# Kernel optimization log

Hardware: AMD Instinct MI355X
Metric: run time of the kernel (lower is better)

The kernel has to match this reference:

```python
import jax, jax.numpy as jnp
import numpy as np
from jax import lax

D = 768          # embed_dim
H = 12           # n_heads
DEPTH = 2
T = 6            # n_timepoints
PS = 7           # patch_size
IMG = (56, 49, 49)
GRID = (8, 7, 7)
NPATCH = 392     # prod(GRID), must be even for the sinusoidal PE
SEQ = T * NPATCH # 2352 space-time tokens
MLP_H = 3072     # int(768 * 4.0)
B = 2
RRELU_MLP = 0.4        # eval-mode RReLU(0.1, 0.7) slope
RRELU_HEAD = 11.0/48.0 # eval-mode RReLU(1/8, 1/3) slope


def _ln(x, g, b, eps=1e-6):
    m = x.mean(-1, keepdims=True)
    v = ((x - m) ** 2).mean(-1, keepdims=True)
    return (x - m) / jnp.sqrt(v + eps) * g + b


def _pos_enc(t, d):
    pos = np.arange(t, dtype=np.float32)[:, None]
    div = 1.0 / 10000.0 ** (np.arange(0, d, 2, dtype=np.float32) / d)
    pe = np.zeros((t, d), np.float32)
    pe[:, 0::2] = np.sin(pos * div)
    pe[:, 1::2] = np.cos(pos * div)
    return jnp.asarray(pe)


def _convT_dw(x, w, bias, stride, dilation):
    # depthwise ConvTranspose3d(C, C, k, stride, dilation, groups=C); w: (C,1,k,k,k)
    C = x.shape[1]
    k = w.shape[-1]
    wf = jnp.flip(w, axis=(2, 3, 4))
    pad = (k - 1) * dilation
    y = lax.conv_general_dilated(
        x, wf, window_strides=(1, 1, 1), padding=[(pad, pad)] * 3,
        lhs_dilation=(stride,) * 3, rhs_dilation=(dilation,) * 3,
        dimension_numbers=('NCDHW', 'OIDHW', 'NCDHW'), feature_group_count=C)
    return y + bias[None, :, None, None, None]


def _nearest(x, size):
    # torch F.interpolate(mode='nearest'): src = floor(dst * in/out)
    for ax, s in zip((2, 3, 4), size):
        idx = (jnp.arange(s) * (x.shape[ax] / s)).astype(jnp.int32)
        x = jnp.take(x, idx, axis=ax)
    return x


def setup_inputs() -> dict:
    key = jax.random.key(0)
    ks = iter(jax.random.split(key, 64))
    def rn(shape, s=0.02):
        return jax.random.normal(next(ks), shape, jnp.float32) * s
    inp = {}
    inp['x'] = jax.random.normal(next(ks), (B, 1, T) + IMG, jnp.float32)
    inp['pconv_w'] = rn((D, 1, PS, PS, PS)); inp['pconv_b'] = rn((D,))
    inp['pos_embed'] = rn((1, SEQ, D))
    inp['ln1_g'] = jnp.ones((DEPTH, D)); inp['ln1_b'] = jnp.zeros((DEPTH, D))
    inp['qkv_w'] = rn((DEPTH, 3 * D, D)); inp['qkv_b'] = rn((DEPTH, 3 * D))
    inp['proj_w'] = rn((DEPTH, D, D)); inp['proj_b'] = rn((DEPTH, D))
    inp['ln2_g'] = jnp.ones((DEPTH, D)); inp['ln2_b'] = jnp.zeros((DEPTH, D))
    inp['fc1_w'] = rn((DEPTH, MLP_H, D)); inp['fc1_b'] = rn((DEPTH, MLP_H))
    inp['fc2_w'] = rn((DEPTH, D, MLP_H)); inp['fc2_b'] = rn((DEPTH, D))
    inp['normf_g'] = jnp.ones((D,)); inp['normf_b'] = jnp.zeros((D,))
    inp['dfc_w'] = rn((1, D)); inp['dfc_b'] = rn((1,))
    inp['up1_w'] = rn((T, 1, 7, 7, 7)); inp['up1_b'] = rn((T,))
    inp['up2_w'] = rn((T, 1, 5, 5, 5)); inp['up2_b'] = rn((T,))
    inp['up3_w'] = rn((T, 1, 9, 9, 9)); inp['up3_b'] = rn((T,))
    inp['hconv_w'] = rn((T, 1, 1, 1, 1)); inp['hconv_b'] = rn((T,))
    return inp


def reference(x, pconv_w, pconv_b, pos_embed, ln1_g, ln1_b, qkv_w, qkv_b,
              proj_w, proj_b, ln2_g, ln2_b, fc1_w, fc1_b, fc2_w, fc2_b,
              normf_g, normf_b, dfc_w, dfc_b, up1_w, up1_b, up2_w, up2_b,
              up3_w, up3_b, hconv_w, hconv_b):
    b = x.shape[0]
    hd = D // H
    scale = hd ** -0.5
    # fold time into batch, patch-embed each 3D frame
    xt = x.transpose(0, 2, 1, 3, 4, 5).reshape(b * T, 1, *IMG)
    y = lax.conv_general_dilated(
        xt, pconv_w, (PS, PS, PS), 'VALID',
        dimension_numbers=('NCDHW', 'OIDHW', 'NCDHW'))
    y = y + pconv_b[None, :, None, None, None]
    tok = y.reshape(b * T, D, NPATCH).transpose(0, 2, 1).reshape(b, SEQ, D)
    tok = tok + pos_embed
    for i in range(DEPTH):
        h = _ln(tok, ln1_g[i], ln1_b[i])
        qkv = (h @ qkv_w[i].T + qkv_b[i]).reshape(b, SEQ, 3, H, hd)
        qkv = qkv.transpose(2, 0, 3, 1, 4)  # (3,b,H,SEQ,hd)
        q, k, v = qkv[0], qkv[1], qkv[2]
        attn = jax.nn.softmax(jnp.einsum('bhnd,bhmd->bhnm', q, k) * scale, axis=-1)
        o = jnp.einsum('bhnm,bhmd->bhnd', attn, v)
        o = o.transpose(0, 2, 1, 3).reshape(b, SEQ, D)
        tok = tok + (o @ proj_w[i].T + proj_b[i])
        h = _ln(tok, ln2_g[i], ln2_b[i])
        h = h @ fc1_w[i].T + fc1_b[i]
        h = jnp.where(h >= 0, h, RRELU_MLP * h)
        tok = tok + (h @ fc2_w[i].T + fc2_b[i])
    tok = _ln(tok, normf_g, normf_b)
    z = tok.reshape(b, T, NPATCH, D)
    # --- DecoderHead ---
    z = (z @ dfc_w.T + dfc_b)[..., 0]           # (b,T,NPATCH)
    z = z - z.mean(axis=1, keepdims=True)       # subtract time mean
    z = z + _pos_enc(T, NPATCH)
    z = z.reshape(b, T, *GRID)                  # (b,T,8,7,7)
    z = _convT_dw(z, up1_w, up1_b, 1, 1)        # -> (b,T,14,13,13)
    z = _convT_dw(z, up2_w, up2_b, 2, 1)        # -> (b,T,31,29,29)
    z = _convT_dw(z, up3_w, up3_b, 1, 2)        # -> (b,T,47,45,45)
    z = _nearest(z, IMG)                        # -> (b,T,56,49,49)
    z = z * hconv_w[:, 0, 0, 0, 0][None, :, None, None, None] \
        + hconv_b[None, :, None, None, None]
    z = jnp.where(z >= 0, z, RRELU_HEAD * z)
    return z[:, None].transpose(0, 1, 3, 4, 5, 2)  # (b,1,56,49,49,T)
```

## Files before the change

kernel.cpp:

```cpp
#include <hip/hip_runtime.h>


#define AS1 __attribute__((address_space(1)))
#define AS3 __attribute__((address_space(3)))

using bf16 = __bf16;
typedef __bf16 bf16x8 __attribute__((ext_vector_type(8)));
typedef float  f32x4  __attribute__((ext_vector_type(4)));

#define CDIV(a, b) (((a) + (b) - 1) / (b))

__device__ __forceinline__ void gll16(const void* g, void* l) {
  __builtin_amdgcn_global_load_lds((AS1 void*)(void*)g, (AS3 void*)l, 16, 0, 0);
}

template <int SH>
__device__ __forceinline__ float rorf(float x) {
  int i = __builtin_amdgcn_update_dpp(0, __builtin_bit_cast(int, x),
                                      0x120 + SH, 0xF, 0xF, false);
  return __builtin_bit_cast(float, i);
}
__device__ __forceinline__ float rowsum16(float v) {
  v += rorf<1>(v); v += rorf<2>(v); v += rorf<4>(v); v += rorf<8>(v);
  return v;
}

__global__ __launch_bounds__(256) void gemm_bt(
    const bf16* __restrict__ A, const bf16* __restrict__ B,
    float* Cf, bf16* Cb, const float* __restrict__ bias,
    const float* addp, int addmod, int rrelu,
    int M, int N, int K, int lda, int ldb, int ldc,
    long long sA, long long sB, long long sC, int ksplit,
    bf16* __restrict__ Qo, bf16* __restrict__ Ko, bf16* __restrict__ Vo) {
  __shared__ __align__(16) bf16 As[2][128 * 32];
  __shared__ __align__(16) bf16 Bs[2][128 * 32];
  const int tid  = threadIdx.x;
  const int lane = tid & 63;
  const int wave = tid >> 6;
  const int wm = wave & 1;
  const int wn = wave >> 1;
  const int q  = lane >> 4;
  const int r  = lane & 15;

  const int nwg = gridDim.x * gridDim.y;
  int flat = blockIdx.y * gridDim.x + blockIdx.x;
  {
    const int qq = nwg >> 3, rr = nwg & 7;
    const int xcd = flat & 7, lid = flat >> 3;
    flat = (xcd < rr ? xcd * (qq + 1) : rr * (qq + 1) + (xcd - rr) * qq) + lid;
  }
  const int tm0 = (flat % gridDim.x) * 128;
  const int tn0 = (flat / gridDim.x) * 128;
  const int z   = blockIdx.z;

  const bf16* Ab = A + (ksplit > 1 ? 0 : (size_t)z * (size_t)sA);
  const bf16* Bb = B + (ksplit > 1 ? 0 : (size_t)z * (size_t)sB);
  int kb = 0, ke = K;
  if (ksplit > 1) {
    const int kc = ((K / ksplit + 31) / 32) * 32;
    kb = z * kc;
    ke = min(kb + kc, K);
  }

  const int arow0 = min(tm0 + (tid >> 2), M - 1);
  const int arow1 = min(tm0 + (tid >> 2) + 64, M - 1);
  const int brow0 = min(tn0 + (tid >> 2), N - 1);
  const int brow1 = min(tn0 + (tid >> 2) + 64, N - 1);
  const int kcol  = (tid & 3) * 8;
  const bf16* ap0 = Ab + (size_t)arow0 * lda + kcol;
  const bf16* ap1 = Ab + (size_t)arow1 * lda + kcol;
  const bf16* bp0 = Bb + (size_t)brow0 * ldb + kcol;
  const bf16* bp1 = Bb + (size_t)brow1 * ldb + kcol;

  f32x4 acc[4][4];
#pragma unroll
  for (int mi = 0; mi < 4; ++mi)
#pragma unroll
    for (int ni = 0; ni < 4; ++ni) acc[mi][ni] = (f32x4){0.f, 0.f, 0.f, 0.f};

  auto stage = [&](int buf, int k0) {
    bf16* as = &As[buf][wave * 512];
    bf16* bs = &Bs[buf][wave * 512];
    gll16(ap0 + k0, as);
    gll16(ap1 + k0, as + 2048);
    gll16(bp0 + k0, bs);
    gll16(bp1 + k0, bs + 2048);
  };

  stage(0, kb);
  int t = 0;
  for (int k0 = kb; k0 < ke; k0 += 32, ++t) {
    const int cur = t & 1;
    __syncthreads();
    if (k0 + 32 < ke) stage(cur ^ 1, k0 + 32);
    bf16x8 af[4], bfr[4];
#pragma unroll
    for (int mi = 0; mi < 4; ++mi)
      af[mi] = *(const bf16x8*)&As[cur][(wm * 64 + mi * 16 + r) * 32 + q * 8];
#pragma unroll
    for (int ni = 0; ni < 4; ++ni)
      bfr[ni] = *(const bf16x8*)&Bs[cur][(wn * 64 + ni * 16 + r) * 32 + q * 8];
#pragma unroll
    for (int mi = 0; mi < 4; ++mi)
#pragma unroll
      for (int ni = 0; ni < 4; ++ni)
        acc[mi][ni] = __builtin_amdgcn_mfma_f32_16x16x32_bf16(
            af[mi], bfr[ni], acc[mi][ni], 0, 0, 0);
  }

  float* cf = Cf ? Cf + (ksplit > 1 ? 0 : (size_t)z * (size_t)sC) : nullptr;
  bf16*  cb = Cb ? Cb + (ksplit > 1 ? 0 : (size_t)z * (size_t)sC) : nullptr;
#pragma unroll
  for (int mi = 0; mi < 4; ++mi) {
    const int row0 = tm0 + wm * 64 + mi * 16 + q * 4;
#pragma unroll
    for (int ni = 0; ni < 4; ++ni) {
      const int col = tn0 + wn * 64 + ni * 16 + r;
      if (col >= N) continue;
      const float bv = bias ? bias[col] : 0.f;
#pragma unroll
      for (int reg = 0; reg < 4; ++reg) {
        const int rr = row0 + reg;
        if (rr >= M) continue;
        if (Qo) {
          const float v = acc[mi][ni][reg] + bv;
          const int which = col / 768;
          const int hh = (col % 768) >> 6;
          const int dd = col & 63;
          const int bb2 = rr / 2352;
          const int ss = rr - bb2 * 2352;
          const int inst = bb2 * 12 + hh;
          if (which == 0)
            Qo[((size_t)inst * 2432 + ss) * 64 + dd] = (bf16)v;
          else if (which == 1)
            Ko[((size_t)inst * 2368 + ss) * 64 + dd] = (bf16)(v * 0.18033688f);
          else
            Vo[((size_t)inst * 64 + dd) * 2368 + ss] = (bf16)v;
        } else if (ksplit > 1) {
          float v = acc[mi][ni][reg];
          if (z == 0) {
            v += bv;
            if (addp) v += addp[(size_t)(rr % addmod) * ldc + col];
          }
          atomicAdd(&cf[(size_t)rr * ldc + col], v);
        } else {
          float v = acc[mi][ni][reg] + bv;
          if (addp) v += addp[(size_t)(rr % addmod) * ldc + col];
          if (rrelu) v = (v >= 0.f) ? v : 0.4f * v;
          if (cf) cf[(size_t)rr * ldc + col] = v;
          else    cb[(size_t)rr * ldc + col] = (bf16)v;
        }
      }
    }
  }
}

__global__ __launch_bounds__(256) void flash_attn_split(
    const bf16* __restrict__ Qg, const bf16* __restrict__ Kg,
    const bf16* __restrict__ Vt, float* __restrict__ Opart,
    float* __restrict__ Lpart) {
  __shared__ __align__(16) bf16 Kl[64 * 64];
  __shared__ __align__(16) bf16 Vl[64 * 64];
  __shared__ __align__(16) bf16 Plds[4][2][16 * 72];
  const int lane = threadIdx.x & 63;
  const int wave = threadIdx.x >> 6;
  const int q = lane >> 4, r = lane & 15;
  const int inst = blockIdx.y;
  const int z = blockIdx.z;
  const int rt_raw = blockIdx.x * 4 + wave;
  const int rt = min(rt_raw, 73);
  const int row0 = rt * 32;
  const int ch0 = (z * 37) >> 1;
  const int ch1 = ((z + 1) * 37) >> 1;
  const bf16* Qi = Qg + (size_t)inst * 2432 * 64;
  const bf16* Ki = Kg + (size_t)inst * 2368 * 64;
  const bf16* Vi = Vt + (size_t)inst * 64 * 2368;

  bf16x8 qf[2][2];
#pragma unroll
  for (int t = 0; t < 2; ++t) {
    qf[t][0] = *(const bf16x8*)&Qi[(size_t)(row0 + t * 16 + r) * 64 + q * 8];
    qf[t][1] = *(const bf16x8*)&Qi[(size_t)(row0 + t * 16 + r) * 64 + 32 + q * 8];
  }

  f32x4 O[2][4];
  float l[2][4];
#pragma unroll
  for (int t = 0; t < 2; ++t)
#pragma unroll
    for (int i = 0; i < 4; ++i) {
      O[t][i] = (f32x4){0.f, 0.f, 0.f, 0.f};
      l[t][i] = 0.f;
    }

  const int rl = lane >> 3;
  const int ul = lane & 7;
  const int swz = (r & 7);

  for (int ch = ch0; ch < ch1; ++ch) {
    const int col0 = ch * 64;
    __syncthreads();
#pragma unroll
    for (int j = 0; j < 2; ++j) {
      const int g = wave * 2 + j;
      const int row = g * 8 + rl;
      const int ug = ul ^ (row & 7);
      gll16(Ki + ((size_t)(col0 + row) * 64 + ug * 8), &Kl[g * 512]);
      gll16(Vi + (size_t)row * 2368 + col0 + ug * 8, &Vl[g * 512]);
    }
    __syncthreads();

    bf16x8 kf0[4], kf1[4], vf0[4], vf1[4];
#pragma unroll
    for (int ct = 0; ct < 4; ++ct) {
      const int krow = ct * 16 + r;
      kf0[ct] = *(const bf16x8*)&Kl[krow * 64 + ((q ^ swz) * 8)];
      kf1[ct] = *(const bf16x8*)&Kl[krow * 64 + (((q + 4) ^ swz) * 8)];
      vf0[ct] = *(const bf16x8*)&Vl[krow * 64 + ((q ^ swz) * 8)];
      vf1[ct] = *(const bf16x8*)&Vl[krow * 64 + (((q + 4) ^ swz) * 8)];
    }

    f32x4 s[2][4];
#pragma unroll
    for (int ct = 0; ct < 4; ++ct) {
#pragma unroll
      for (int t = 0; t < 2; ++t) {
        f32x4 a = (f32x4){0.f, 0.f, 0.f, 0.f};
        a = __builtin_amdgcn_mfma_f32_16x16x32_bf16(qf[t][0], kf0[ct], a, 0, 0, 0);
        a = __builtin_amdgcn_mfma_f32_16x16x32_bf16(qf[t][1], kf1[ct], a, 0, 0, 0);
        s[t][ct] = a;
      }
    }
    if (ch == 36) {
      s[0][3] = (f32x4){-1e30f, -1e30f, -1e30f, -1e30f};
      s[1][3] = (f32x4){-1e30f, -1e30f, -1e30f, -1e30f};
    }
#pragma unroll
    for (int t = 0; t < 2; ++t) {
      float csum[4] = {0.f, 0.f, 0.f, 0.f};
#pragma unroll
      for (int ct = 0; ct < 4; ++ct)
#pragma unroll
        for (int reg = 0; reg < 4; ++reg) {
          float p = exp2f(s[t][ct][reg]);
          s[t][ct][reg] = p;
          csum[reg] += p;
        }
#pragma unroll
      for (int reg = 0; reg < 4; ++reg)
        l[t][reg] += rowsum16(csum[reg]);
      bf16* Pw = Plds[wave][t];
#pragma unroll
      for (int ct = 0; ct < 4; ++ct)
#pragma unroll
        for (int reg = 0; reg < 4; ++reg)
          Pw[(q * 4 + reg) * 72 + ct * 16 + r] = (bf16)s[t][ct][reg];
    }
#pragma unroll
    for (int t = 0; t < 2; ++t) {
      const bf16* Pw = Plds[wave][t];
      const bf16x8 pf0 = *(const bf16x8*)&Pw[r * 72 + q * 8];
      const bf16x8 pf1 = *(const bf16x8*)&Pw[r * 72 + 32 + q * 8];
#pragma unroll
      for (int ot = 0; ot < 4; ++ot) {
        O[t][ot] = __builtin_amdgcn_mfma_f32_16x16x32_bf16(pf0, vf0[ot], O[t][ot], 0, 0, 0);
        O[t][ot] = __builtin_amdgcn_mfma_f32_16x16x32_bf16(pf1, vf1[ot], O[t][ot], 0, 0, 0);
      }
    }
  }
  if (rt_raw < 74) {
#pragma unroll
    for (int t = 0; t < 2; ++t) {
      const int p = (z * 24 + inst) * 152 + rt * 2 + t;
      float* Op = Opart + (size_t)p * 1024;
#pragma unroll
      for (int ot = 0; ot < 4; ++ot)
#pragma unroll
        for (int reg = 0; reg < 4; ++reg)
          Op[(q * 4 + reg) * 64 + ot * 16 + r] = O[t][ot][reg];
      if (r == 0) {
#pragma unroll
        for (int reg = 0; reg < 4; ++reg)
          Lpart[(size_t)p * 16 + q * 4 + reg] = l[t][reg];
      }
    }
  }
}

__global__ __launch_bounds__(256) void attn_combine(
    const float* __restrict__ Opart, const float* __restrict__ Lpart,
    bf16* __restrict__ Og) {
  const int tile = blockIdx.x;
  const int inst = blockIdx.y;
  const int bb = inst / 12, hh = inst % 12;
  const int pb = inst * 152 + tile;
#pragma unroll
  for (int i = 0; i < 4; ++i) {
    const int e = threadIdx.x + 256 * i;
    const int row = e >> 6, col = e & 63;
    const float lsum = Lpart[(size_t)pb * 16 + row] +
                       Lpart[(size_t)(3648 + pb) * 16 + row];
    const float osum = Opart[(size_t)pb * 1024 + e] +
                       Opart[(size_t)(3648 + pb) * 1024 + e];
    Og[(size_t)(bb * 2352 + tile * 16 + row) * 768 + hh * 64 + col] =
        (bf16)(osum / lsum);
  }
}


__global__ void zero_pads(bf16* __restrict__ Q, bf16* __restrict__ Kb,
                          bf16* __restrict__ VT) {
  int i = blockIdx.x * 256 + threadIdx.x;
  if (i < 122880) {
    int inst = i / 5120, rem = i % 5120;
    Q[((size_t)inst * 2432 + 2352 + rem / 64) * 64 + (rem & 63)] = (bf16)0.f;
  }
  if (i < 24576) {
    int inst = i / 1024, rem = i % 1024;
    Kb[((size_t)inst * 2368 + 2352 + rem / 64) * 64 + (rem & 63)] = (bf16)0.f;
  }
  if (i < 24576) {
    int inst = i / 1024, rem = i % 1024;
    VT[((size_t)inst * 64 + rem / 16) * 2368 + 2352 + (rem & 15)] = (bf16)0.f;
  }
}

__global__ void cvt_bf16(const float* __restrict__ x, bf16* __restrict__ y, int n) {
  int i = blockIdx.x * 256 + threadIdx.x;
  if (i < n) y[i] = (bf16)x[i];
}

__global__ void prep_pconv(const float* __restrict__ w, bf16* __restrict__ y) {
  int i = blockIdx.x * 256 + threadIdx.x;
  if (i >= 768 * 352) return;
  int d = i / 352, j = i % 352;
  y[i] = (bf16)(j < 343 ? w[d * 343 + j] : 0.f);
}

__global__ void im2col(const float* __restrict__ x, bf16* __restrict__ A) {
  int i = blockIdx.x * 256 + threadIdx.x;
  if (i >= 4704 * 352) return;
  int j = i % 352, tok = i / 352;
  float v = 0.f;
  if (j < 343) {
    int p = tok % 392, bt = tok / 392;
    int kx = j % 7, ky = (j / 7) % 7, kz = j / 49;
    int px = p % 7, py = (p / 7) % 7, pz = p / 49;
    int zz = pz * 7 + kz, yy = py * 7 + ky, xx = px * 7 + kx;
    v = x[(((size_t)bt * 56 + zz) * 49 + yy) * 49 + xx];
  }
  A[i] = (bf16)v;
}

template <typename OT>
__global__ __launch_bounds__(256) void ln_kernel(
    const float* __restrict__ x, const float* __restrict__ g,
    const float* __restrict__ bb, OT* __restrict__ y, int M) {
  int row = blockIdx.x * 4 + (threadIdx.x >> 6);
  int lane = threadIdx.x & 63;
  if (row >= M) return;
  const float* xr = x + (size_t)row * 768;
  float v[12], s = 0.f;
#pragma unroll
  for (int i = 0; i < 12; ++i) { v[i] = xr[lane + i * 64]; s += v[i]; }
#pragma unroll
  for (int off = 32; off; off >>= 1) s += __shfl_xor(s, off, 64);
  float mean = s * (1.f / 768.f);
  float vs = 0.f;
#pragma unroll
  for (int i = 0; i < 12; ++i) { float d = v[i] - mean; vs += d * d; }
#pragma unroll
  for (int off = 32; off; off >>= 1) vs += __shfl_xor(vs, off, 64);
  float inv = 1.f / sqrtf(vs * (1.f / 768.f) + 1e-6f);
#pragma unroll
  for (int i = 0; i < 12; ++i) {
    int j = lane + i * 64;
    y[(size_t)row * 768 + j] = (OT)((v[i] - mean) * inv * g[j] + bb[j]);
  }
}

__global__ __launch_bounds__(256) void dfc_kernel(
    const float* __restrict__ x, const float* __restrict__ w,
    const float* __restrict__ b0, float* __restrict__ z0, int M) {
  int row = blockIdx.x * 4 + (threadIdx.x >> 6);
  int lane = threadIdx.x & 63;
  if (row >= M) return;
  const float* xr = x + (size_t)row * 768;
  float s = 0.f;
#pragma unroll
  for (int i = 0; i < 12; ++i) s += xr[lane + i * 64] * w[lane + i * 64];
#pragma unroll
  for (int off = 32; off; off >>= 1) s += __shfl_xor(s, off, 64);
  if (lane == 0) z0[row] = s + b0[0];
}

__global__ void head_pe(const float* __restrict__ z0, float* __restrict__ z1) {
  int i = blockIdx.x * 256 + threadIdx.x;
  if (i >= 784) return;
  int b = i / 392, p = i % 392;
  float vals[6], m = 0.f;
#pragma unroll
  for (int t = 0; t < 6; ++t) { vals[t] = z0[(b * 6 + t) * 392 + p]; m += vals[t]; }
  m *= (1.f / 6.f);
  float e = (float)(2 * (p >> 1)) / 392.0f;
  float div = powf(10000.f, -e);
#pragma unroll
  for (int t = 0; t < 6; ++t) {
    float arg = (float)t * div;
    float pe = (p & 1) ? cosf(arg) : sinf(arg);
    z1[(b * 6 + t) * 392 + p] = vals[t] - m + pe;
  }
}

template <int ID, int IH, int IW, int PD, int PH, int PWA, int OFF, int ST>
__global__ void pad_in(const float* __restrict__ x, float* __restrict__ Xp) {
  int i = blockIdx.x * 256 + threadIdx.x;
  constexpr int total = 12 * PD * PH * PWA;
  if (i >= total) return;
  int px = i % PWA, t1 = i / PWA;
  int py = t1 % PH, t2 = t1 / PH;
  int pz = t2 % PD, c = t2 / PD;
  float v = 0.f;
  int tz = pz - OFF, ty = py - OFF, tx = px - OFF;
  if (tz >= 0 && ty >= 0 && tx >= 0 &&
      (ST == 1 || (((tz | ty | tx) & 1) == 0))) {
    int iz = tz / ST, iy = ty / ST, ix = tx / ST;
    if (iz < ID && iy < IH && ix < IW)
      v = x[((size_t)(c * ID + iz) * IH + iy) * IW + ix];
  }
  Xp[i] = v;
}

template <int PD, int PH, int PWA, int OD, int OH, int OW, int K, int DIL>
__global__ __launch_bounds__(256) void convt4(
    const float* __restrict__ Xp, const float* __restrict__ w,
    const float* __restrict__ bias, float* __restrict__ y) {
  constexpr int P0  = (K - 1) * DIL;
  constexpr int QX  = (OW + 3) / 4;
  constexpr int NLD = (P0 + 4 + 3) / 4;
  int idx = blockIdx.x * 256 + threadIdx.x;
  if (idx >= OD * OH * QX) return;
  int c = blockIdx.y;
  int qx = idx % QX; int t1 = idx / QX;
  int oy = t1 % OH;  int oz = t1 / OH;
  int ox0 = qx * 4;
  const float* xc = Xp + (size_t)c * (PD * PH * PWA);
  const float* wc = w + (c % 6) * (K * K * K);
  const float bv = bias[c % 6];
  float a0 = bv, a1 = bv, a2 = bv, a3 = bv;
  for (int kz = 0; kz < K; ++kz) {
    const int bz = oz + P0 - kz * DIL;
#pragma unroll
    for (int ky = 0; ky < K; ++ky) {
      const int by = oy + P0 - ky * DIL;
      const float* base = xc + ((size_t)bz * PH + by) * PWA + ox0;
      float buf[NLD * 4];
#pragma unroll
      for (int i = 0; i < NLD; ++i)
        *(f32x4*)&buf[i * 4] = *(const f32x4*)(base + i * 4);
      const float* wr = wc + (kz * K + ky) * K;
#pragma unroll
      for (int kx = 0; kx < K; ++kx) {
        const float wv = wr[kx];
        const int j = P0 - kx * DIL;
        a0 += wv * buf[j + 0];
        a1 += wv * buf[j + 1];
        a2 += wv * buf[j + 2];
        a3 += wv * buf[j + 3];
      }
    }
  }
  float* yp = y + (size_t)c * (OD * OH * OW) + ((size_t)oz * OH + oy) * OW + ox0;
  yp[0] = a0;
  if (ox0 + 1 < OW) yp[1] = a1;
  if (ox0 + 2 < OW) yp[2] = a2;
  if (ox0 + 3 < OW) yp[3] = a3;
}

__global__ void head_final(const float* __restrict__ z4, const float* __restrict__ hw,
                           const float* __restrict__ hb, float* __restrict__ out) {
  int idx = blockIdx.x * 256 + threadIdx.x;
  if (idx >= 1613472) return;
  int t = idx % 6, rdx = idx / 6;
  int xx = rdx % 49; rdx /= 49;
  int yy = rdx % 49; rdx /= 49;
  int zz = rdx % 56; int b = rdx / 56;
  const float rz = (float)(47.0 / 56.0), ry = (float)(45.0 / 49.0);
  int iz = (int)((float)zz * rz);
  int iy = (int)((float)yy * ry);
  int ix = (int)((float)xx * ry);
  float v = z4[(((size_t)(b * 6 + t) * 47 + iz) * 45 + iy) * 45 + ix];
  v = v * hw[t] + hb[t];
  v = (v >= 0.f) ? v : (11.0f / 48.0f) * v;
  out[idx] = v;
}


static inline void launch_gemm(hipStream_t s, const bf16* A, const bf16* B,
                               float* Cf, bf16* Cb, const float* bias,
                               const float* addp, int addmod, int rrelu,
                               int M, int N, int K, int lda, int ldb, int ldc,
                               long long sA, long long sB, long long sC,
                               int nz, int ksplit = 1,
                               bf16* Qo = nullptr, bf16* Ko = nullptr,
                               bf16* Vo = nullptr) {
  dim3 g(CDIV(M, 128), CDIV(N, 128), ksplit > 1 ? ksplit : nz);
  gemm_bt<<<g, 256, 0, s>>>(A, B, Cf, Cb, bias, addp, addmod, rrelu,
                            M, N, K, lda, ldb, ldc, sA, sB, sC, ksplit,
                            Qo, Ko, Vo);
}

extern "C" void kernel_launch(void* const* d_in, const int* in_sizes, int n_in,
                              void* d_out, int out_size, void* d_ws, size_t ws_size,
                              hipStream_t stream) {
  (void)in_sizes; (void)n_in; (void)out_size; (void)ws_size;
  const float* x       = (const float*)d_in[0];
  const float* pconv_w = (const float*)d_in[1];
  const float* pconv_b = (const float*)d_in[2];
  const float* pos_emb = (const float*)d_in[3];
  const float* ln1_g   = (const float*)d_in[4];
  const float* ln1_b   = (const float*)d_in[5];
  const float* qkv_wf  = (const float*)d_in[6];
  const float* qkv_b   = (const float*)d_in[7];
  const float* proj_wf = (const float*)d_in[8];
  const float* proj_b  = (const float*)d_in[9];
  const float* ln2_g   = (const float*)d_in[10];
  const float* ln2_b   = (const float*)d_in[11];
  const float* fc1_wf  = (const float*)d_in[12];
  const float* fc1_b   = (const float*)d_in[13];
  const float* fc2_wf  = (const float*)d_in[14];
  const float* fc2_b   = (const float*)d_in[15];
  const float* normf_g = (const float*)d_in[16];
  const float* normf_b = (const float*)d_in[17];
  const float* dfc_w   = (const float*)d_in[18];
  const float* dfc_b   = (const float*)d_in[19];
  const float* up1_w   = (const float*)d_in[20];
  const float* up1_b   = (const float*)d_in[21];
  const float* up2_w   = (const float*)d_in[22];
  const float* up2_b   = (const float*)d_in[23];
  const float* up3_w   = (const float*)d_in[24];
  const float* up3_b   = (const float*)d_in[25];
  const float* hconv_w = (const float*)d_in[26];
  const float* hconv_b = (const float*)d_in[27];
  float* out = (float*)d_out;

  char* ws = (char*)d_ws;
  size_t off = 0;
  auto alloc = [&](size_t bytes) -> void* {
    void* p = ws + off;
    off += (bytes + 255) & ~(size_t)255;
    return p;
  };
  float* tok   = (float*)alloc(4704UL * 768 * 4);
  bf16* lnout  = (bf16*)alloc(4704UL * 768 * 2);
  bf16* Qb     = (bf16*)alloc(24UL * 2432 * 64 * 2);
  bf16* Kb     = (bf16*)alloc(24UL * 2368 * 64 * 2);
  bf16* VT     = (bf16*)alloc(24UL * 64 * 2368 * 2);
  bf16* attnb  = (bf16*)alloc(4704UL * 768 * 2);
  bf16* hb     = (bf16*)alloc(4704UL * 3072 * 2);
  bf16* Apatch = (bf16*)alloc(4704UL * 352 * 2);
  bf16* Wq     = (bf16*)alloc(2UL * 2304 * 768 * 2);
  bf16* Wp     = (bf16*)alloc(2UL * 768 * 768 * 2);
  bf16* W1     = (bf16*)alloc(2UL * 3072 * 768 * 2);
  bf16* W2     = (bf16*)alloc(2UL * 768 * 3072 * 2);
  bf16* Wpc    = (bf16*)alloc(768UL * 352 * 2);
  float* Opart = (float*)alloc(2UL * 24 * 152 * 1024 * 4);
  float* Lpart = (float*)alloc(2UL * 24 * 152 * 16 * 4);
  float* z0    = (float*)alloc(4704UL * 4);
  float* z1    = (float*)alloc(4704UL * 4);
  float* z2    = (float*)alloc(12UL * 14 * 13 * 13 * 4);
  float* z3    = (float*)alloc(12UL * 31 * 29 * 29 * 4);
  float* z4    = (float*)alloc(12UL * 47 * 45 * 45 * 4);
  float* p1    = (float*)alloc(12UL * 20 * 19 * 24 * 4);
  float* p2    = (float*)alloc(12UL * 35 * 33 * 36 * 4);
  float* p3    = (float*)alloc(12UL * 63 * 61 * 64 * 4);
  float* lnf   = (float*)alloc(4704UL * 768 * 4);

  cvt_bf16<<<CDIV(3538944, 256), 256, 0, stream>>>(qkv_wf, Wq, 3538944);
  cvt_bf16<<<CDIV(1179648, 256), 256, 0, stream>>>(proj_wf, Wp, 1179648);
  cvt_bf16<<<CDIV(4718592, 256), 256, 0, stream>>>(fc1_wf, W1, 4718592);
  cvt_bf16<<<CDIV(4718592, 256), 256, 0, stream>>>(fc2_wf, W2, 4718592);
  prep_pconv<<<CDIV(768 * 352, 256), 256, 0, stream>>>(pconv_w, Wpc);
  zero_pads<<<CDIV(122880, 256), 256, 0, stream>>>(Qb, Kb, VT);

  im2col<<<CDIV(4704 * 352, 256), 256, 0, stream>>>(x, Apatch);
  launch_gemm(stream, Apatch, Wpc, tok, nullptr, pconv_b, pos_emb, 2352, 0,
              4704, 768, 352, 352, 352, 768, 0, 0, 0, 1);

  for (int i = 0; i < 2; ++i) {
    ln_kernel<bf16><<<1176, 256, 0, stream>>>(tok, ln1_g + i * 768, ln1_b + i * 768, lnout, 4704);
    launch_gemm(stream, lnout, Wq + (size_t)i * 2304 * 768, nullptr, nullptr,
                qkv_b + i * 2304, nullptr, 1, 0,
                4704, 2304, 768, 768, 768, 2304, 0, 0, 0, 1, 1, Qb, Kb, VT);
    flash_attn_split<<<dim3(19, 24, 2), 256, 0, stream>>>(Qb, Kb, VT, Opart, Lpart);
    attn_combine<<<dim3(147, 24), 256, 0, stream>>>(Opart, Lpart, attnb);
    launch_gemm(stream, attnb, Wp + (size_t)i * 768 * 768, tok, nullptr,
                proj_b + i * 768, nullptr, 1, 0,
                4704, 768, 768, 768, 768, 768, 0, 0, 0, 1, 4);
    ln_kernel<bf16><<<1176, 256, 0, stream>>>(tok, ln2_g + i * 768, ln2_b + i * 768, lnout, 4704);
    launch_gemm(stream, lnout, W1 + (size_t)i * 3072 * 768, nullptr, hb,
                fc1_b + i * 3072, nullptr, 1, 1,
                4704, 3072, 768, 768, 768, 3072, 0, 0, 0, 1);
    launch_gemm(stream, hb, W2 + (size_t)i * 768 * 3072, tok, nullptr,
                fc2_b + i * 768, nullptr, 1, 0,
                4704, 768, 3072, 3072, 3072, 768, 0, 0, 0, 1, 4);
  }

  ln_kernel<float><<<1176, 256, 0, stream>>>(tok, normf_g, normf_b, lnf, 4704);
  dfc_kernel<<<1176, 256, 0, stream>>>(lnf, dfc_w, dfc_b, z0, 4704);
  head_pe<<<4, 256, 0, stream>>>(z0, z1);

  pad_in<8, 7, 7, 20, 19, 24, 6, 1>
      <<<CDIV(12 * 20 * 19 * 24, 256), 256, 0, stream>>>(z1, p1);
  convt4<20, 19, 24, 14, 13, 13, 7, 1>
      <<<dim3(CDIV(14 * 13 * 4, 256), 12), 256, 0, stream>>>(p1, up1_w, up1_b, z2);
  pad_in<14, 13, 13, 35, 33, 36, 4, 2>
      <<<CDIV(12 * 35 * 33 * 36, 256), 256, 0, stream>>>(z2, p2);
  convt4<35, 33, 36, 31, 29, 29, 5, 1>
      <<<dim3(CDIV(31 * 29 * 8, 256), 12), 256, 0, stream>>>(p2, up2_w, up2_b, z3);
  pad_in<31, 29, 29, 63, 61, 64, 16, 1>
      <<<CDIV(12 * 63 * 61 * 64, 256), 256, 0, stream>>>(z3, p3);
  convt4<63, 61, 64, 47, 45, 45, 9, 2>
      <<<dim3(CDIV(47 * 45 * 12, 256), 12), 256, 0, stream>>>(p3, up3_w, up3_b, z4);

  head_final<<<CDIV(1613472, 256), 256, 0, stream>>>(z4, hconv_w, hconv_b, out);
}
```

Before: 1.078 ms.

## Register-prefetch next K/V chunk in flash attention instead of direct global-to-LDS loads

Replaces the synchronous global_load_lds copies of each K/V chunk with register loads that fetch the next chunk while the current one is computed. The staged registers are written to LDS at the top of each iteration, between barriers. This is meant to hide global-memory latency behind the MFMA work, and launch bounds now request 4 blocks per CU. The cost is extra VGPRs for the staging registers, which together with the occupancy hint could cause register pressure or spills.

```diff
diff --git a/kernel.cpp b/kernel.cpp
--- a/kernel.cpp
+++ b/kernel.cpp
@@ -155,15 +155,16 @@
   }
 }
 
-__global__ __launch_bounds__(256) void flash_attn_split(
+__global__ __launch_bounds__(256, 4) void flash_attn_split(
     const bf16* __restrict__ Qg, const bf16* __restrict__ Kg,
     const bf16* __restrict__ Vt, float* __restrict__ Opart,
     float* __restrict__ Lpart) {
   __shared__ __align__(16) bf16 Kl[64 * 64];
   __shared__ __align__(16) bf16 Vl[64 * 64];
   __shared__ __align__(16) bf16 Plds[4][2][16 * 72];
-  const int lane = threadIdx.x & 63;
-  const int wave = threadIdx.x >> 6;
+  const int tid  = threadIdx.x;
+  const int lane = tid & 63;
+  const int wave = tid >> 6;
   const int q = lane >> 4, r = lane & 15;
   const int inst = blockIdx.y;
   const int z = blockIdx.z;
@@ -193,22 +194,39 @@
       l[t][i] = 0.f;
     }
 
-  const int rl = lane >> 3;
-  const int ul = lane & 7;
+  const int srow = tid >> 3;
+  const int suc  = tid & 7;
+  const int gu   = (suc ^ (srow & 7)) * 8;
+  bf16* const kd0 = &Kl[srow * 64 + suc * 8];
+  bf16* const kd1 = &Kl[(srow + 32) * 64 + suc * 8];
+  bf16* const vd0 = &Vl[srow * 64 + suc * 8];
+  bf16* const vd1 = &Vl[(srow + 32) * 64 + suc * 8];
   const int swz = (r & 7);
 
+  bf16x8 kr0, kr1, vr0, vr1;
+  auto loadKV = [&](int ch) {
+    const size_t col0 = (size_t)ch * 64;
+    kr0 = *(const bf16x8*)&Ki[(col0 + srow) * 64 + gu];
+    kr1 = *(const bf16x8*)&Ki[(col0 + srow + 32) * 64 + gu];
+    vr0 = *(const bf16x8*)&Vi[(size_t)srow * 2368 + col0 + gu];
+    vr1 = *(const bf16x8*)&Vi[(size_t)(srow + 32) * 2368 + col0 + gu];
+  };
+
+  loadKV(ch0);
   for (int ch = ch0; ch < ch1; ++ch) {
-    const int col0 = ch * 64;
-    __syncthreads();
-#pragma unroll
-    for (int j = 0; j < 2; ++j) {
-      const int g = wave * 2 + j;
-      const int row = g * 8 + rl;
-      const int ug = ul ^ (row & 7);
-      gll16(Ki + ((size_t)(col0 + row) * 64 + ug * 8), &Kl[g * 512]);
-      gll16(Vi + (size_t)row * 2368 + col0 + ug * 8, &Vl[g * 512]);
-    }
-    __syncthreads();
+    asm volatile("s_waitcnt lgkmcnt(0)" ::: "memory");
+    __builtin_amdgcn_sched_barrier(0);
+    __builtin_amdgcn_s_barrier();
+    asm volatile("" ::: "memory");
+    *(bf16x8*)kd0 = kr0;
+    *(bf16x8*)kd1 = kr1;
+    *(bf16x8*)vd0 = vr0;
+    *(bf16x8*)vd1 = vr1;
+    if (ch + 1 < ch1) loadKV(ch + 1);
+    asm volatile("s_waitcnt lgkmcnt(0)" ::: "memory");
+    __builtin_amdgcn_sched_barrier(0);
+    __builtin_amdgcn_s_barrier();
+    asm volatile("" ::: "memory");
 
     bf16x8 kf0[4], kf1[4], vf0[4], vf1[4];
 #pragma unroll
```

New measurement: 1.101 ms. +2.1%, slower.
